# Kernel optimization log

Hardware: AMD Instinct MI355X
Metric: run time of the kernel (lower is better)

Reference implementation:

```python
import jax, jax.numpy as jnp
import numpy as np

N_WIN = 7
DIM = 128
QK = 128
HEADS = 8
TOPK = 4


def _win(x, n_win):
    # (N, H, W, C) -> (N, n_win*n_win, h, w, C)
    N, H, W, C = x.shape
    h, w = H // n_win, W // n_win
    return x.reshape(N, n_win, h, n_win, w, C).transpose(0, 1, 3, 2, 4, 5).reshape(N, n_win * n_win, h, w, C)


def _unwin(x, n_win):
    # (N, p2, h, w, C) -> (N, H, W, C)
    N, p2, h, w, C = x.shape
    return x.reshape(N, n_win, n_win, h, w, C).transpose(0, 1, 3, 2, 4, 5).reshape(N, n_win * h, n_win * w, C)


def _dwconv(img_nhwc, k, b):
    # depthwise 3x3, SAME padding (LePE)
    x = img_nhwc.transpose(0, 3, 1, 2)
    y = jax.lax.conv_general_dilated(x, k, (1, 1), 'SAME',
                                     dimension_numbers=('NCHW', 'OIHW', 'NCHW'),
                                     feature_group_count=k.shape[0])
    y = y + b[None, :, None, None]
    return y.transpose(0, 2, 3, 1)


def _branch(xw, W, b):
    # xw: (N, p2, h, w, C); QKV linear + pixel/window-level views
    qkv = xw @ W + b
    q, kv = qkv[..., :QK], qkv[..., QK:]
    N, p2, h, w, _ = q.shape
    q_pix = q.reshape(N, p2, h * w, QK)
    kv_pix = kv.reshape(N, p2, h * w, QK + DIM)  # identity kv_down
    q_win = q.mean((2, 3))
    k_win = kv[..., :QK].mean((2, 3))
    return q_pix, kv_pix, q_win, k_win, kv


def _route(q_win, k_win, scale):
    # non-differentiable routing (detach) with Identity emb
    q = jax.lax.stop_gradient(q_win)
    k = jax.lax.stop_gradient(k_win)
    logit = (q * scale) @ k.transpose(0, 2, 1)  # (N, p2, p2)
    top_val, top_idx = jax.lax.top_k(logit, TOPK)
    r_weight = jax.nn.softmax(top_val, axis=-1)  # unused (mul_weight='none')
    return r_weight, top_idx


def _gather(kv_pix, idx):
    # kv_pix: (N, p2, w2, c), idx: (N, p2, K) -> (N, p2, K, w2, c)
    N = kv_pix.shape[0]
    bidx = jnp.arange(N)[:, None, None]
    return kv_pix[bidx, idx]


def _heads_q(q):
    # (N, p2, w2, m*c) -> (N, p2, m, w2, c)
    N, p2, w2, _ = q.shape
    return q.reshape(N, p2, w2, HEADS, -1).transpose(0, 1, 3, 2, 4)


def _heads_kv(kv):
    # (N, p2, K, w2, m*c) -> (N, p2, m, K*w2, c)
    N, p2, K, w2, _ = kv.shape
    return kv.reshape(N, p2, K, w2, HEADS, -1).transpose(0, 1, 4, 2, 3, 5).reshape(N, p2, HEADS, K * w2, -1)


def setup_inputs() -> dict:
    key = jax.random.key(0)
    ks = jax.random.split(key, 6)
    N, H, W = 8, 56, 56
    return {
        'x': jax.random.normal(ks[0], (N, H, W, DIM), jnp.float32),
        'y': jax.random.normal(ks[1], (N, H, W, DIM), jnp.float32),
        'w_qkv_x': jax.random.normal(ks[2], (DIM, 2 * QK + DIM), jnp.float32) * 0.02,
        'b_qkv_x': jnp.zeros((2 * QK + DIM,), jnp.float32),
        'w_qkv_y': jax.random.normal(ks[3], (DIM, 2 * QK + DIM), jnp.float32) * 0.02,
        'b_qkv_y': jnp.zeros((2 * QK + DIM,), jnp.float32),
        'w_lepe_x': jax.random.normal(ks[4], (DIM, 1, 3, 3), jnp.float32) * 0.1,
        'b_lepe_x': jnp.zeros((DIM,), jnp.float32),
        'w_lepe_y': jax.random.normal(ks[5], (DIM, 1, 3, 3), jnp.float32) * 0.1,
        'b_lepe_y': jnp.zeros((DIM,), jnp.float32),
    }


def reference(x, y, w_qkv_x, b_qkv_x, w_qkv_y, b_qkv_y, w_lepe_x, b_lepe_x, w_lepe_y, b_lepe_y):
    scale = QK ** (-0.5)
    N, H, W, C = x.shape
    h, w = H // N_WIN, W // N_WIN
    xw = _win(x, N_WIN)
    yw = _win(y, N_WIN)

    qx_pix, kvx_pix, qx_win, kx_win, kvx = _branch(xw, w_qkv_x, b_qkv_x)
    qy_pix, kvy_pix, qy_win, ky_win, kvy = _branch(yw, w_qkv_y, b_qkv_y)

    lepe_x = _dwconv(_unwin(kvx[..., QK:], N_WIN), w_lepe_x, b_lepe_x)
    lepe_y = _dwconv(_unwin(kvy[..., QK:], N_WIN), w_lepe_y, b_lepe_y)

    _, rx_idx = _route(qx_win, kx_win, scale)
    _, ry_idx = _route(qy_win, ky_win, scale)

    kvx_sel = _gather(kvx_pix, rx_idx)  # (N, p2, K, w2, QK+DIM)
    kvy_sel = _gather(kvy_pix, ry_idx)

    kx_sel, vx_sel = _heads_kv(kvx_sel[..., :QK]), _heads_kv(kvx_sel[..., QK:])
    ky_sel, vy_sel = _heads_kv(kvy_sel[..., :QK]), _heads_kv(kvy_sel[..., QK:])
    qx = _heads_q(qx_pix)
    qy = _heads_q(qy_pix)

    attn_x = jax.nn.softmax(jnp.einsum('bpmqc,bpmkc->bpmqk', qx * scale, kx_sel), axis=-1)
    attn_y = jax.nn.softmax(jnp.einsum('bpmqc,bpmkc->bpmqk', qy * scale, ky_sel), axis=-1)

    # cross attention: x-output uses y's attention weights on x's values, and vice versa
    out_x = jnp.einsum('bpmqk,bpmkc->bpmqc', attn_y, vx_sel)
    out_y = jnp.einsum('bpmqk,bpmkc->bpmqc', attn_x, vy_sel)

    p2 = N_WIN * N_WIN
    out_x = out_x.transpose(0, 1, 3, 2, 4).reshape(N, p2, h, w, DIM)
    out_y = out_y.transpose(0, 1, 3, 2, 4).reshape(N, p2, h, w, DIM)
    out_x = _unwin(out_x, N_WIN) + lepe_x
    out_y = _unwin(out_y, N_WIN) + lepe_y
    return (out_x, out_y)
```

## Files before the change

kernel.cpp:

```cpp
#include <hip/hip_runtime.h>

#define HWD 56
#define NWIN 7
#define P2 49
#define CIN 128
#define COUT 384
#define NB 8
#define SCALE 0.08838834764831843f

typedef __attribute__((ext_vector_type(8))) short bf16x8;
typedef __attribute__((ext_vector_type(4))) float f32x4;
typedef __attribute__((ext_vector_type(8))) unsigned short u16x8;
typedef unsigned short ushort_t;

__device__ inline unsigned short f2bf(float f) {
  unsigned int u = __float_as_uint(f);
  unsigned int r = (u + 0x7fffu + ((u >> 16) & 1u)) >> 16;
  return (unsigned short)r;
}
__device__ inline float bf2f(unsigned short b) {
  return __uint_as_float(((unsigned int)b) << 16);
}

__global__ __launch_bounds__(256) void meanproj_kernel(
    const float* __restrict__ xin, const float* __restrict__ yin,
    const float* __restrict__ Wx, const float* __restrict__ Bx,
    const float* __restrict__ Wy, const float* __restrict__ By,
    ushort_t* __restrict__ xbfx, ushort_t* __restrict__ xbfy,
    float* __restrict__ qwx, float* __restrict__ kwx,
    float* __restrict__ qwy, float* __restrict__ kwy)
{
  const int p = blockIdx.x, n = blockIdx.y, br = blockIdx.z;
  const float* X  = br ? yin : xin;
  const float* W  = br ? Wy  : Wx;
  const float* Bv = br ? By  : Bx;
  ushort_t* xb = (br ? xbfy : xbfx) + (size_t)(n * P2 + p) * 64 * CIN;
  float* qw = br ? qwy : qwx;
  float* kw = br ? kwy : kwx;

  __shared__ float sm[2][128];
  __shared__ float mxs[128];
  const int t = threadIdx.x;
  const int wr = p / NWIN, wc = p % NWIN;
  const int ch = t & 127, half = t >> 7;

  float s = 0.f;
#pragma unroll 4
  for (int i = 0; i < 32; ++i) {
    int pix = half * 32 + i;
    int a = wr * 8 + (pix >> 3), b = wc * 8 + (pix & 7);
    float v = X[(((size_t)n * HWD + a) * HWD + b) * CIN + ch];
    s += v;
    xb[pix * CIN + ch] = f2bf(v);
  }
  sm[half][ch] = s;
  __syncthreads();
  if (t < 128) mxs[t] = (sm[0][t] + sm[1][t]) * (1.f / 64.f);
  __syncthreads();

  float acc = Bv[t];
#pragma unroll 8
  for (int k = 0; k < 128; ++k) acc = fmaf(mxs[k], W[(size_t)k * COUT + t], acc);
  if (t < 128) qw[(n * P2 + p) * 128 + t] = acc;
  else         kw[(n * P2 + p) * 128 + (t - 128)] = acc;
}

__global__ __launch_bounds__(128) void wt_kernel(
    const float* __restrict__ Wx, const float* __restrict__ Wy,
    ushort_t* __restrict__ Wtx, ushort_t* __restrict__ Wty)
{
  const int br = blockIdx.y;
  const float* W = br ? Wy : Wx;
  ushort_t* Wt = br ? Wty : Wtx;
  const int c = blockIdx.x * 128 + threadIdx.x;
  for (int k8 = 0; k8 < 128; k8 += 8) {
    u16x8 buf;
#pragma unroll
    for (int i = 0; i < 8; ++i) buf[i] = f2bf(W[(size_t)(k8 + i) * COUT + c]);
    *(u16x8*)&Wt[(size_t)c * 128 + k8] = buf;
  }
}

__global__ __launch_bounds__(256) void route_kernel(
    const float* __restrict__ qwx, const float* __restrict__ kwx,
    const float* __restrict__ qwy, const float* __restrict__ kwy,
    int* __restrict__ idxx, int* __restrict__ idxy)
{
  const int br = blockIdx.x, n = blockIdx.y;
  const float* qw = br ? qwy : qwx;
  const float* kw = br ? kwy : kwx;
  int* idx = br ? idxy : idxx;

  __shared__ float qs[P2][128];
  __shared__ float ks[P2][128];
  __shared__ float ls[P2][52];
  const int t = threadIdx.x;
  for (int e = t; e < P2 * 128; e += 256) {
    qs[e >> 7][e & 127] = qw[(size_t)n * P2 * 128 + e];
    ks[e >> 7][e & 127] = kw[(size_t)n * P2 * 128 + e];
  }
  __syncthreads();
  for (int pair = t; pair < P2 * P2; pair += 256) {
    int r = pair / P2, j = pair % P2;
    float d = 0.f;
#pragma unroll
    for (int c4 = 0; c4 < 32; ++c4) {
      float4 a = *(const float4*)&qs[r][c4 * 4];
      float4 b = *(const float4*)&ks[j][c4 * 4];
      d = fmaf(a.x, b.x, d); d = fmaf(a.y, b.y, d);
      d = fmaf(a.z, b.z, d); d = fmaf(a.w, b.w, d);
    }
    ls[r][j] = d;
  }
  __syncthreads();
  if (t < P2) {
    int ch[4];
    for (int s = 0; s < 4; ++s) {
      float best = -1e30f; int bi = 0;
      for (int j = 0; j < P2; ++j) {
        bool taken = false;
        for (int u = 0; u < s; ++u) taken = taken || (ch[u] == j);
        if (!taken && ls[t][j] > best) { best = ls[t][j]; bi = j; }
      }
      ch[s] = bi;
      idx[((size_t)n * P2 + t) * 4 + s] = bi;
    }
  }
}

#define AS 136
__global__ __launch_bounds__(256) void qkv_gemm_kernel(
    const ushort_t* __restrict__ xbfx, const ushort_t* __restrict__ xbfy,
    const ushort_t* __restrict__ Wtx, const ushort_t* __restrict__ Wty,
    const float* __restrict__ Bx, const float* __restrict__ By,
    ushort_t* __restrict__ qkvx, ushort_t* __restrict__ qkvy)
{
  const int mt = blockIdx.x, nt = blockIdx.y, br = blockIdx.z;
  const ushort_t* Xb = br ? xbfy : xbfx;
  const ushort_t* Wt = br ? Wty : Wtx;
  const float* Bv = br ? By : Bx;
  ushort_t* out = br ? qkvy : qkvx;

  __shared__ ushort_t a_s[128 * AS];
  __shared__ ushort_t b_s[128 * AS];

  const int t = threadIdx.x;
#pragma unroll
  for (int it = 0; it < 8; ++it) {
    int row = it * 16 + (t >> 4);
    int e8 = (t & 15) * 8;
    *(u16x8*)&a_s[row * AS + e8] = *(const u16x8*)&Xb[((size_t)mt * 128 + row) * 128 + e8];
    *(u16x8*)&b_s[row * AS + e8] = *(const u16x8*)&Wt[((size_t)nt * 128 + row) * 128 + e8];
  }
  __syncthreads();

  const int wv = t >> 6, wm = wv >> 1, wn = wv & 1;
  const int lane = t & 63, qd = lane >> 4, m16 = lane & 15;

  f32x4 acc[4][4];
#pragma unroll
  for (int i = 0; i < 4; ++i)
#pragma unroll
    for (int j = 0; j < 4; ++j) acc[i][j] = (f32x4){0.f, 0.f, 0.f, 0.f};

#pragma unroll
  for (int ks = 0; ks < 4; ++ks) {
    bf16x8 af[4], bfr[4];
#pragma unroll
    for (int fi = 0; fi < 4; ++fi)
      af[fi] = *(const bf16x8*)&a_s[(wm * 64 + fi * 16 + m16) * AS + ks * 32 + qd * 8];
#pragma unroll
    for (int fj = 0; fj < 4; ++fj)
      bfr[fj] = *(const bf16x8*)&b_s[(wn * 64 + fj * 16 + m16) * AS + ks * 32 + qd * 8];
#pragma unroll
    for (int fi = 0; fi < 4; ++fi)
#pragma unroll
      for (int fj = 0; fj < 4; ++fj)
        acc[fi][fj] = __builtin_amdgcn_mfma_f32_16x16x32_bf16(bfr[fj], af[fi], acc[fi][fj], 0, 0, 0);
  }

  const float scl = (nt == 0) ? SCALE : 1.0f;
#pragma unroll
  for (int fj = 0; fj < 4; ++fj) {
    int chb = nt * 128 + wn * 64 + fj * 16 + qd * 4;
    float4 b4 = *(const float4*)&Bv[chb];
#pragma unroll
    for (int fi = 0; fi < 4; ++fi) {
      int tok = wm * 64 + fi * 16 + m16;
      ushort4 st = {f2bf((acc[fi][fj][0] + b4.x) * scl), f2bf((acc[fi][fj][1] + b4.y) * scl),
                    f2bf((acc[fi][fj][2] + b4.z) * scl), f2bf((acc[fi][fj][3] + b4.w) * scl)};
      *(ushort4*)&out[((size_t)mt * 128 + tok) * COUT + chb] = st;
    }
  }
}

#define KR 24
__global__ __launch_bounds__(256) void attn_kernel(
    const ushort_t* __restrict__ qkvx, const ushort_t* __restrict__ qkvy,
    const int* __restrict__ idxx, const int* __restrict__ idxy,
    const float* __restrict__ wlx, const float* __restrict__ blx,
    const float* __restrict__ wly, const float* __restrict__ bly,
    float* __restrict__ dout)
{
  const int p = blockIdx.x, n = blockIdx.y, z = blockIdx.z;
  const int h = z >> 1, dir = z & 1;
  const ushort_t* qkvQ = dir ? qkvy : qkvx;
  const ushort_t* qkvV = dir ? qkvx : qkvy;
  const int* idxK = dir ? idxy : idxx;
  const int* idxV = dir ? idxx : idxy;
  const float* wl = dir ? wlx : wly;
  const float* bl = dir ? blx : bly;
  const size_t OUTHALF = (size_t)NB * HWD * HWD * CIN;
  float* outp = dout + (dir ? 0 : OUTHALF);

  __shared__ ushort_t kb[256 * KR];
  __shared__ ushort_t qb[64 * KR];
  __shared__ ushort_t vt[16 * 264];
  __shared__ float halo[100 * 20];
  __shared__ float wls[160];

  const int t = threadIdx.x;
  const int wv = t >> 6, r = t & 63;
  const int wr = p / NWIN, wc = p % NWIN;

  const int kwin = idxK[((size_t)n * P2 + p) * 4 + wv];
  const int vwin = idxV[((size_t)n * P2 + p) * 4 + wv];

  {
    const ushort_t* src = qkvQ + ((size_t)(n * P2 + kwin) * 64 + r) * COUT + 128 + h * 16;
    *(u16x8*)&kb[t * KR] = *(const u16x8*)src;
    *(u16x8*)&kb[t * KR + 8] = *(const u16x8*)(src + 8);
  }
  if (t < 64) {
    const ushort_t* src = qkvQ + ((size_t)(n * P2 + p) * 64 + t) * COUT + h * 16;
    *(u16x8*)&qb[t * KR] = *(const u16x8*)src;
    *(u16x8*)&qb[t * KR + 8] = *(const u16x8*)(src + 8);
  }
  {
    const ushort_t* src = qkvV + ((size_t)(n * P2 + vwin) * 64 + r) * COUT + 256 + h * 16;
    u16x8 v0 = *(const u16x8*)src;
    u16x8 v1 = *(const u16x8*)(src + 8);
#pragma unroll
    for (int c = 0; c < 8; ++c) {
      vt[c * 264 + wv * 64 + r] = v0[c];
      vt[(c + 8) * 264 + wv * 64 + r] = v1[c];
    }
  }
  if (t < 200) {
    int hp = t >> 1, hf = t & 1;
    int A = wr * 8 - 1 + (int)((unsigned)hp / 10u);
    int B = wc * 8 - 1 + (int)((unsigned)hp % 10u);
    f32x4 f0 = {0.f, 0.f, 0.f, 0.f}, f1 = {0.f, 0.f, 0.f, 0.f};
    if ((unsigned)A < (unsigned)HWD && (unsigned)B < (unsigned)HWD) {
      int gw = (A >> 3) * NWIN + (B >> 3);
      int pix = (A & 7) * 8 + (B & 7);
      u16x8 vv = *(const u16x8*)(qkvV + ((size_t)(n * P2 + gw) * 64 + pix) * COUT + 256 + h * 16 + hf * 8);
      f0[0] = bf2f(vv[0]); f0[1] = bf2f(vv[1]); f0[2] = bf2f(vv[2]); f0[3] = bf2f(vv[3]);
      f1[0] = bf2f(vv[4]); f1[1] = bf2f(vv[5]); f1[2] = bf2f(vv[6]); f1[3] = bf2f(vv[7]);
    }
    *(f32x4*)&halo[hp * 20 + hf * 8] = f0;
    *(f32x4*)&halo[hp * 20 + hf * 8 + 4] = f1;
  }
  if (t < 160) {
    int row = t >> 4, c = t & 15;
    wls[t] = (row < 9) ? wl[(h * 16 + c) * 9 + row] : bl[h * 16 + c];
  }
  __syncthreads();

  const int qd = r >> 4, m16 = r & 15;
  const f32x4 zf = {0.f, 0.f, 0.f, 0.f};

  bf16x8 qf = (bf16x8)(short)0;
  if (qd < 2) qf = *(const bf16x8*)&qb[(wv * 16 + m16) * KR + qd * 8];

  f32x4 s[8][2];
#pragma unroll
  for (int c = 0; c < 8; ++c) {
    bf16x8 kf0 = (bf16x8)(short)0, kf1 = (bf16x8)(short)0;
    if (qd < 2) {
      kf0 = *(const bf16x8*)&kb[(c * 32 + m16) * KR + qd * 8];
      kf1 = *(const bf16x8*)&kb[(c * 32 + 16 + m16) * KR + qd * 8];
    }
    s[c][0] = __builtin_amdgcn_mfma_f32_16x16x32_bf16(kf0, qf, zf, 0, 0, 0);
    s[c][1] = __builtin_amdgcn_mfma_f32_16x16x32_bf16(kf1, qf, zf, 0, 0, 0);
  }

  float m = -1e30f;
#pragma unroll
  for (int c = 0; c < 8; ++c)
#pragma unroll
    for (int hh = 0; hh < 2; ++hh)
#pragma unroll
      for (int rr = 0; rr < 4; ++rr) m = fmaxf(m, s[c][hh][rr]);
  m = fmaxf(m, __shfl_xor(m, 16));
  m = fmaxf(m, __shfl_xor(m, 32));
  float l = 0.f;
#pragma unroll
  for (int c = 0; c < 8; ++c)
#pragma unroll
    for (int hh = 0; hh < 2; ++hh)
#pragma unroll
      for (int rr = 0; rr < 4; ++rr) {
        float e = __expf(s[c][hh][rr] - m);
        s[c][hh][rr] = e;
        l += e;
      }
  l += __shfl_xor(l, 16);
  l += __shfl_xor(l, 32);
  const float inv = 1.f / l;

  f32x4 oacc = {0.f, 0.f, 0.f, 0.f};
#pragma unroll
  for (int c = 0; c < 8; ++c) {
    int pk[4];
#pragma unroll
    for (int rr = 0; rr < 4; ++rr)
      pk[rr] = (int)((unsigned int)f2bf(s[c][0][rr]) | ((unsigned int)f2bf(s[c][1][rr]) << 16));
    u16x8 pfu;
#pragma unroll
    for (int j = 0; j < 8; ++j) {
      int srcl = (((qd & 1) * 2 + (j >> 2)) << 4) + m16;
      int w = __shfl(pk[j & 3], srcl);
      pfu[j] = (qd < 2) ? (unsigned short)(w & 0xffff) : (unsigned short)((unsigned)w >> 16);
    }
    bf16x8 vtf = *(const bf16x8*)&vt[m16 * 264 + c * 32 + qd * 8];
    oacc = __builtin_amdgcn_mfma_f32_16x16x32_bf16(vtf, *(bf16x8*)&pfu, oacc, 0, 0, 0);
  }

  const int pix = wv * 16 + m16;
  const int pa = pix >> 3, pb = pix & 7;

  f32x4 lep = *(const f32x4*)&wls[144 + qd * 4];
#pragma unroll
  for (int di = 0; di < 3; ++di)
#pragma unroll
    for (int dj = 0; dj < 3; ++dj) {
      f32x4 hv = *(const f32x4*)&halo[((pa + di) * 10 + pb + dj) * 20 + qd * 4];
      f32x4 wt4 = *(const f32x4*)&wls[(di * 3 + dj) * 16 + qd * 4];
#pragma unroll
      for (int rr = 0; rr < 4; ++rr) lep[rr] = fmaf(hv[rr], wt4[rr], lep[rr]);
    }

  const int ga = wr * 8 + pa, gb = wc * 8 + pb;
  float4 o = {oacc[0] * inv + lep[0], oacc[1] * inv + lep[1],
              oacc[2] * inv + lep[2], oacc[3] * inv + lep[3]};
  *(float4*)&outp[(((size_t)n * HWD + ga) * HWD + gb) * CIN + h * 16 + qd * 4] = o;
}

extern "C" void kernel_launch(void* const* d_in, const int* in_sizes, int n_in,
                              void* d_out, int out_size, void* d_ws, size_t ws_size,
                              hipStream_t stream) {
  const float* x        = (const float*)d_in[0];
  const float* y        = (const float*)d_in[1];
  const float* w_qkv_x  = (const float*)d_in[2];
  const float* b_qkv_x  = (const float*)d_in[3];
  const float* w_qkv_y  = (const float*)d_in[4];
  const float* b_qkv_y  = (const float*)d_in[5];
  const float* w_lepe_x = (const float*)d_in[6];
  const float* b_lepe_x = (const float*)d_in[7];
  const float* w_lepe_y = (const float*)d_in[8];
  const float* b_lepe_y = (const float*)d_in[9];
  float* out = (float*)d_out;

  const size_t qkv_sz = (size_t)NB * P2 * 64 * COUT;
  const size_t xbf_sz = (size_t)NB * P2 * 64 * CIN;
  const size_t wt_sz  = (size_t)COUT * CIN;
  const size_t win_sz = (size_t)NB * P2 * 128;

  ushort_t* qkvx = (ushort_t*)d_ws;
  ushort_t* qkvy = qkvx + qkv_sz;
  ushort_t* xbfx = qkvy + qkv_sz;
  ushort_t* xbfy = xbfx + xbf_sz;
  ushort_t* Wtx  = xbfy + xbf_sz;
  ushort_t* Wty  = Wtx + wt_sz;
  float* qwx = (float*)(Wty + wt_sz);
  float* kwx = qwx + win_sz;
  float* qwy = kwx + win_sz;
  float* kwy = qwy + win_sz;
  int* idxx = (int*)(kwy + win_sz);
  int* idxy = idxx + NB * P2 * 4;

  meanproj_kernel<<<dim3(P2, NB, 2), 256, 0, stream>>>(
      x, y, w_qkv_x, b_qkv_x, w_qkv_y, b_qkv_y, xbfx, xbfy, qwx, kwx, qwy, kwy);
  wt_kernel<<<dim3(3, 2), 128, 0, stream>>>(w_qkv_x, w_qkv_y, Wtx, Wty);
  route_kernel<<<dim3(2, NB), 256, 0, stream>>>(qwx, kwx, qwy, kwy, idxx, idxy);
  qkv_gemm_kernel<<<dim3(196, 3, 2), 256, 0, stream>>>(
      xbfx, xbfy, Wtx, Wty, b_qkv_x, b_qkv_y, qkvx, qkvy);
  attn_kernel<<<dim3(P2, NB, 16), 256, 0, stream>>>(
      qkvx, qkvy, idxx, idxy, w_lepe_x, b_lepe_x, w_lepe_y, b_lepe_y, out);
}
```

Baseline: 244.7 us.

## Write QKV in head-major per-window layouts and read attention operands directly from global

The QKV GEMM epilogue now writes Q, K and V into per-window, per-head contiguous buffers, plus a channel-major transposed copy of V, in place of one interleaved token-major QKV tensor. The attention kernel loads MFMA fragments for Q, K and V straight from global memory and drops the LDS staging buffers for them, keeping shared memory only for the LePE halo and weights. The barrier moves after the attention math so the halo loads can overlap the matrix work. In exchange the GEMM writes an extra V copy with scattered 2-byte stores, and fragment loads now go to global memory through cache instead of LDS.

```diff
diff --git a/kernel.cpp b/kernel.cpp
--- a/kernel.cpp
+++ b/kernel.cpp
@@ -133,13 +133,15 @@
     const ushort_t* __restrict__ xbfx, const ushort_t* __restrict__ xbfy,
     const ushort_t* __restrict__ Wtx, const ushort_t* __restrict__ Wty,
     const float* __restrict__ Bx, const float* __restrict__ By,
-    ushort_t* __restrict__ qkvx, ushort_t* __restrict__ qkvy)
+    ushort_t* __restrict__ Qpx, ushort_t* __restrict__ Qpy,
+    ushort_t* __restrict__ Kpx, ushort_t* __restrict__ Kpy,
+    ushort_t* __restrict__ Vcx, ushort_t* __restrict__ Vcy,
+    ushort_t* __restrict__ Vpx, ushort_t* __restrict__ Vpy)
 {
   const int mt = blockIdx.x, nt = blockIdx.y, br = blockIdx.z;
   const ushort_t* Xb = br ? xbfy : xbfx;
   const ushort_t* Wt = br ? Wty : Wtx;
   const float* Bv = br ? By : Bx;
-  ushort_t* out = br ? qkvy : qkvx;
 
   __shared__ ushort_t a_s[128 * AS];
   __shared__ ushort_t b_s[128 * AS];
@@ -179,24 +181,54 @@
         acc[fi][fj] = __builtin_amdgcn_mfma_f32_16x16x32_bf16(bfr[fj], af[fi], acc[fi][fj], 0, 0, 0);
   }
 
+  const int gw = mt * 2 + wm;
   const float scl = (nt == 0) ? SCALE : 1.0f;
-#pragma unroll
-  for (int fj = 0; fj < 4; ++fj) {
-    int chb = nt * 128 + wn * 64 + fj * 16 + qd * 4;
-    float4 b4 = *(const float4*)&Bv[chb];
-#pragma unroll
-    for (int fi = 0; fi < 4; ++fi) {
-      int tok = wm * 64 + fi * 16 + m16;
-      ushort4 st = {f2bf((acc[fi][fj][0] + b4.x) * scl), f2bf((acc[fi][fj][1] + b4.y) * scl),
-                    f2bf((acc[fi][fj][2] + b4.z) * scl), f2bf((acc[fi][fj][3] + b4.w) * scl)};
-      *(ushort4*)&out[((size_t)mt * 128 + tok) * COUT + chb] = st;
-    }
-  }
-}
-
-#define KR 24
+
+  if (nt < 2) {
+    ushort_t* dst = (nt == 0) ? (br ? Qpy : Qpx) : (br ? Kpy : Kpx);
+#pragma unroll
+    for (int fj = 0; fj < 4; ++fj) {
+      int lch = wn * 64 + fj * 16 + qd * 4;
+      int h = lch >> 4, chlo = lch & 15;
+      float4 b4 = *(const float4*)&Bv[nt * 128 + lch];
+#pragma unroll
+      for (int fi = 0; fi < 4; ++fi) {
+        int pix = fi * 16 + m16;
+        ushort4 st = {f2bf((acc[fi][fj][0] + b4.x) * scl), f2bf((acc[fi][fj][1] + b4.y) * scl),
+                      f2bf((acc[fi][fj][2] + b4.z) * scl), f2bf((acc[fi][fj][3] + b4.w) * scl)};
+        *(ushort4*)&dst[(((size_t)gw * 8 + h) * 64 + pix) * 16 + chlo] = st;
+      }
+    }
+  } else {
+    ushort_t* dvp = br ? Vpy : Vpx;
+    ushort_t* dvc = br ? Vcy : Vcx;
+#pragma unroll
+    for (int fj = 0; fj < 4; ++fj) {
+      int lch = wn * 64 + fj * 16 + qd * 4;
+      int h = lch >> 4, chlo = lch & 15;
+      float4 b4 = *(const float4*)&Bv[256 + lch];
+#pragma unroll
+      for (int fi = 0; fi < 4; ++fi) {
+        int pix = fi * 16 + m16;
+        float v0 = acc[fi][fj][0] + b4.x, v1 = acc[fi][fj][1] + b4.y;
+        float v2 = acc[fi][fj][2] + b4.z, v3 = acc[fi][fj][3] + b4.w;
+        ushort4 st = {f2bf(v0), f2bf(v1), f2bf(v2), f2bf(v3)};
+        *(ushort4*)&dvp[(((size_t)gw * 8 + h) * 64 + pix) * 16 + chlo] = st;
+        size_t cb = (((size_t)gw * 8 + h) * 16 + chlo) * 64 + pix;
+        dvc[cb]        = st.x;
+        dvc[cb + 64]   = st.y;
+        dvc[cb + 128]  = st.z;
+        dvc[cb + 192]  = st.w;
+      }
+    }
+  }
+}
+
 __global__ __launch_bounds__(256) void attn_kernel(
-    const ushort_t* __restrict__ qkvx, const ushort_t* __restrict__ qkvy,
+    const ushort_t* __restrict__ Qpx, const ushort_t* __restrict__ Qpy,
+    const ushort_t* __restrict__ Kpx, const ushort_t* __restrict__ Kpy,
+    const ushort_t* __restrict__ Vcx, const ushort_t* __restrict__ Vcy,
+    const ushort_t* __restrict__ Vpx, const ushort_t* __restrict__ Vpy,
     const int* __restrict__ idxx, const int* __restrict__ idxy,
     const float* __restrict__ wlx, const float* __restrict__ blx,
     const float* __restrict__ wly, const float* __restrict__ bly,
@@ -204,8 +236,10 @@
 {
   const int p = blockIdx.x, n = blockIdx.y, z = blockIdx.z;
   const int h = z >> 1, dir = z & 1;
-  const ushort_t* qkvQ = dir ? qkvy : qkvx;
-  const ushort_t* qkvV = dir ? qkvx : qkvy;
+  const ushort_t* Qp = dir ? Qpy : Qpx;
+  const ushort_t* Kp = dir ? Kpy : Kpx;
+  const ushort_t* Vc = dir ? Vcx : Vcy;
+  const ushort_t* Vp = dir ? Vpx : Vpy;
   const int* idxK = dir ? idxy : idxx;
   const int* idxV = dir ? idxx : idxy;
   const float* wl = dir ? wlx : wly;
@@ -213,9 +247,6 @@
   const size_t OUTHALF = (size_t)NB * HWD * HWD * CIN;
   float* outp = dout + (dir ? 0 : OUTHALF);
 
-  __shared__ ushort_t kb[256 * KR];
-  __shared__ ushort_t qb[64 * KR];
-  __shared__ ushort_t vt[16 * 264];
   __shared__ float halo[100 * 20];
   __shared__ float wls[160];
 
@@ -223,29 +254,11 @@
   const int wv = t >> 6, r = t & 63;
   const int wr = p / NWIN, wc = p % NWIN;
 
-  const int kwin = idxK[((size_t)n * P2 + p) * 4 + wv];
-  const int vwin = idxV[((size_t)n * P2 + p) * 4 + wv];
-
-  {
-    const ushort_t* src = qkvQ + ((size_t)(n * P2 + kwin) * 64 + r) * COUT + 128 + h * 16;
-    *(u16x8*)&kb[t * KR] = *(const u16x8*)src;
-    *(u16x8*)&kb[t * KR + 8] = *(const u16x8*)(src + 8);
-  }
-  if (t < 64) {
-    const ushort_t* src = qkvQ + ((size_t)(n * P2 + p) * 64 + t) * COUT + h * 16;
-    *(u16x8*)&qb[t * KR] = *(const u16x8*)src;
-    *(u16x8*)&qb[t * KR + 8] = *(const u16x8*)(src + 8);
-  }
-  {
-    const ushort_t* src = qkvV + ((size_t)(n * P2 + vwin) * 64 + r) * COUT + 256 + h * 16;
-    u16x8 v0 = *(const u16x8*)src;
-    u16x8 v1 = *(const u16x8*)(src + 8);
-#pragma unroll
-    for (int c = 0; c < 8; ++c) {
-      vt[c * 264 + wv * 64 + r] = v0[c];
-      vt[(c + 8) * 264 + wv * 64 + r] = v1[c];
-    }
-  }
+  const int4 kidx = *(const int4*)&idxK[((size_t)n * P2 + p) * 4];
+  const int4 vidx = *(const int4*)&idxV[((size_t)n * P2 + p) * 4];
+  const int kw4[4] = {kidx.x, kidx.y, kidx.z, kidx.w};
+  const int vw4[4] = {vidx.x, vidx.y, vidx.z, vidx.w};
+
   if (t < 200) {
     int hp = t >> 1, hf = t & 1;
     int A = wr * 8 - 1 + (int)((unsigned)hp / 10u);
@@ -254,7 +267,7 @@
     if ((unsigned)A < (unsigned)HWD && (unsigned)B < (unsigned)HWD) {
       int gw = (A >> 3) * NWIN + (B >> 3);
       int pix = (A & 7) * 8 + (B & 7);
-      u16x8 vv = *(const u16x8*)(qkvV + ((size_t)(n * P2 + gw) * 64 + pix) * COUT + 256 + h * 16 + hf * 8);
+      u16x8 vv = *(const u16x8*)&Vp[(((size_t)(n * P2 + gw) * 8 + h) * 64 + pix) * 16 + hf * 8];
       f0[0] = bf2f(vv[0]); f0[1] = bf2f(vv[1]); f0[2] = bf2f(vv[2]); f0[3] = bf2f(vv[3]);
       f1[0] = bf2f(vv[4]); f1[1] = bf2f(vv[5]); f1[2] = bf2f(vv[6]); f1[3] = bf2f(vv[7]);
     }
@@ -265,21 +278,23 @@
     int row = t >> 4, c = t & 15;
     wls[t] = (row < 9) ? wl[(h * 16 + c) * 9 + row] : bl[h * 16 + c];
   }
-  __syncthreads();
 
   const int qd = r >> 4, m16 = r & 15;
   const f32x4 zf = {0.f, 0.f, 0.f, 0.f};
 
+  const ushort_t* Qw = Qp + ((size_t)(n * P2 + p) * 8 + h) * 1024;
   bf16x8 qf = (bf16x8)(short)0;
-  if (qd < 2) qf = *(const bf16x8*)&qb[(wv * 16 + m16) * KR + qd * 8];
+  if (qd < 2) qf = *(const bf16x8*)&Qw[(wv * 16 + m16) * 16 + qd * 8];
 
   f32x4 s[8][2];
 #pragma unroll
   for (int c = 0; c < 8; ++c) {
+    const ushort_t* Kw = Kp + ((size_t)(n * P2 + kw4[c >> 1]) * 8 + h) * 1024;
+    int lk = (c & 1) * 32;
     bf16x8 kf0 = (bf16x8)(short)0, kf1 = (bf16x8)(short)0;
     if (qd < 2) {
-      kf0 = *(const bf16x8*)&kb[(c * 32 + m16) * KR + qd * 8];
-      kf1 = *(const bf16x8*)&kb[(c * 32 + 16 + m16) * KR + qd * 8];
+      kf0 = *(const bf16x8*)&Kw[(lk + m16) * 16 + qd * 8];
+      kf1 = *(const bf16x8*)&Kw[(lk + 16 + m16) * 16 + qd * 8];
     }
     s[c][0] = __builtin_amdgcn_mfma_f32_16x16x32_bf16(kf0, qf, zf, 0, 0, 0);
     s[c][1] = __builtin_amdgcn_mfma_f32_16x16x32_bf16(kf1, qf, zf, 0, 0, 0);
@@ -323,9 +338,12 @@
       int w = __shfl(pk[j & 3], srcl);
       pfu[j] = (qd < 2) ? (unsigned short)(w & 0xffff) : (unsigned short)((unsigned)w >> 16);
     }
-    bf16x8 vtf = *(const bf16x8*)&vt[m16 * 264 + c * 32 + qd * 8];
+    const ushort_t* Vw = Vc + ((size_t)(n * P2 + vw4[c >> 1]) * 8 + h) * 1024;
+    bf16x8 vtf = *(const bf16x8*)&Vw[m16 * 64 + (c & 1) * 32 + qd * 8];
     oacc = __builtin_amdgcn_mfma_f32_16x16x32_bf16(vtf, *(bf16x8*)&pfu, oacc, 0, 0, 0);
   }
+
+  __syncthreads();
 
   const int pix = wv * 16 + m16;
   const int pa = pix >> 3, pb = pix & 7;
@@ -362,17 +380,18 @@
   const float* b_lepe_y = (const float*)d_in[9];
   float* out = (float*)d_out;
 
-  const size_t qkv_sz = (size_t)NB * P2 * 64 * COUT;
+  const size_t hb_sz  = (size_t)NB * P2 * 8 * 64 * 16;
   const size_t xbf_sz = (size_t)NB * P2 * 64 * CIN;
   const size_t wt_sz  = (size_t)COUT * CIN;
   const size_t win_sz = (size_t)NB * P2 * 128;
 
-  ushort_t* qkvx = (ushort_t*)d_ws;
-  ushort_t* qkvy = qkvx + qkv_sz;
-  ushort_t* xbfx = qkvy + qkv_sz;
-  ushort_t* xbfy = xbfx + xbf_sz;
-  ushort_t* Wtx  = xbfy + xbf_sz;
-  ushort_t* Wty  = Wtx + wt_sz;
+  ushort_t* base = (ushort_t*)d_ws;
+  ushort_t* Qpx = base;            ushort_t* Qpy = Qpx + hb_sz;
+  ushort_t* Kpx = Qpy + hb_sz;     ushort_t* Kpy = Kpx + hb_sz;
+  ushort_t* Vcx = Kpy + hb_sz;     ushort_t* Vcy = Vcx + hb_sz;
+  ushort_t* Vpx = Vcy + hb_sz;     ushort_t* Vpy = Vpx + hb_sz;
+  ushort_t* xbfx = Vpy + hb_sz;    ushort_t* xbfy = xbfx + xbf_sz;
+  ushort_t* Wtx  = xbfy + xbf_sz;  ushort_t* Wty  = Wtx + wt_sz;
   float* qwx = (float*)(Wty + wt_sz);
   float* kwx = qwx + win_sz;
   float* qwy = kwx + win_sz;
@@ -385,7 +404,9 @@
   wt_kernel<<<dim3(3, 2), 128, 0, stream>>>(w_qkv_x, w_qkv_y, Wtx, Wty);
   route_kernel<<<dim3(2, NB), 256, 0, stream>>>(qwx, kwx, qwy, kwy, idxx, idxy);
   qkv_gemm_kernel<<<dim3(196, 3, 2), 256, 0, stream>>>(
-      xbfx, xbfy, Wtx, Wty, b_qkv_x, b_qkv_y, qkvx, qkvy);
+      xbfx, xbfy, Wtx, Wty, b_qkv_x, b_qkv_y,
+      Qpx, Qpy, Kpx, Kpy, Vcx, Vcy, Vpx, Vpy);
   attn_kernel<<<dim3(P2, NB, 16), 256, 0, stream>>>(
-      qkvx, qkvy, idxx, idxy, w_lepe_x, b_lepe_x, w_lepe_y, b_lepe_y, out);
-}
+      Qpx, Qpy, Kpx, Kpy, Vcx, Vcy, Vpx, Vpy, idxx, idxy,
+      w_lepe_x, b_lepe_x, w_lepe_y, b_lepe_y, out);
+}
```

After: 231.5 us. -5.4%, faster.
